# Optimization experiments

Measured on AMD Instinct MI355X. Metric: run time of the kernel, lower is better.

The kernel has to match this reference:

```python
import jax, jax.numpy as jnp
import numpy as np

B, N, C, H = 2, 2048, 1024, 16
D = C // H  # head_dim = 64


def _rope_freqs(n, d_half, theta=10000.0):
    inv = 1.0 / (theta ** (np.arange(0, d_half, dtype=np.float32) / d_half))
    ang = np.arange(n, dtype=np.float32)[:, None] * inv[None, :]
    return jnp.asarray(np.cos(ang)), jnp.asarray(np.sin(ang))


def setup_inputs() -> dict:
    key = jax.random.key(0)
    ks = jax.random.split(key, 5)
    cos, sin = _rope_freqs(N, D // 2)
    s = 0.02
    return {
        "x": jax.random.normal(ks[0], (B, N, C), jnp.float32),
        "w_qkv": jax.random.normal(ks[1], (3 * C, C), jnp.float32) * s,
        "b_qkv": jnp.zeros((3 * C,), jnp.float32),
        "w_proj": jax.random.normal(ks[2], (C, C), jnp.float32) * s,
        "b_proj": jnp.zeros((C,), jnp.float32),
        "freqs_cos": cos,
        "freqs_sin": sin,
    }


def _apply_rope(t, cos, sin):
    # t: (B, H, N, D); consecutive pairs (even, odd) form complex numbers,
    # matching torch.view_as_complex on reshape(..., D//2, 2).
    te = t[..., 0::2]
    to = t[..., 1::2]
    cos = cos[None, None, :, :]  # (1,1,N,D//2)
    sin = sin[None, None, :, :]
    oe = te * cos - to * sin
    oo = te * sin + to * cos
    return jnp.stack([oe, oo], axis=-1).reshape(t.shape)


def reference(x, w_qkv, b_qkv, w_proj, b_proj, freqs_cos, freqs_sin):
    b, n, c = x.shape
    qkv = x @ w_qkv.T + b_qkv                      # (B,N,3C)
    qkv = qkv.reshape(b, n, 3, H, D).transpose(2, 0, 3, 1, 4)  # (3,B,H,N,D)
    q, k, v = qkv[0], qkv[1], qkv[2]
    q = _apply_rope(q, freqs_cos, freqs_sin)
    k = _apply_rope(k, freqs_cos, freqs_sin)
    scale = 1.0 / jnp.sqrt(jnp.asarray(D, x.dtype))
    scores = jnp.einsum("bhqd,bhkd->bhqk", q, k) * scale
    attn = jax.nn.softmax(scores, axis=-1)
    out = jnp.einsum("bhqk,bhkd->bhqd", attn, v)   # (B,H,N,D)
    out = out.transpose(0, 2, 1, 3).reshape(b, n, c)
    return out @ w_proj.T + b_proj
```

## Files before the change

kernel.cpp:

```cpp
#include <hip/hip_runtime.h>
#include <hip/hip_bf16.h>
#include <stdint.h>

#define BB 2
#define NN 2048
#define CC 1024
#define HH 16
#define DD 64
#define C3 3072

typedef __attribute__((ext_vector_type(8))) short bf16x8;
typedef __attribute__((ext_vector_type(4))) short bf16x4;
typedef __attribute__((ext_vector_type(4))) float f32x4;
typedef __attribute__((ext_vector_type(16))) float f32x16;
typedef __attribute__((ext_vector_type(4))) unsigned short ushort4_t;

__device__ __forceinline__ unsigned short f2bf(float f) {
  union { float f; unsigned u; } v; v.f = f;
  unsigned r = v.u + 0x7FFFu + ((v.u >> 16) & 1u);
  return (unsigned short)(r >> 16);
}

#if __has_builtin(__builtin_amdgcn_exp2f)
#define EXP2(x) __builtin_amdgcn_exp2f(x)
#else
#define EXP2(x) exp2f(x)
#endif

__device__ __forceinline__ unsigned pack_bf2(float a, float b) {
  union { float f; unsigned u; } ua, ub; ua.f = a; ub.f = b;
#if __has_builtin(__builtin_amdgcn_perm)
  return __builtin_amdgcn_perm(ub.u, ua.u, 0x07060302u);
#else
  return (ua.u >> 16) | (ub.u & 0xFFFF0000u);
#endif
}

#define QSCALE 0.18033688f

#define GLDS(g, l) __builtin_amdgcn_global_load_lds( \
    (const __attribute__((address_space(1))) void*)(g), \
    (__attribute__((address_space(3))) void*)(l), 16, 0, 0)

__global__ __launch_bounds__(256) void k_cvt(
    const float* __restrict__ x, const float* __restrict__ wq,
    const float* __restrict__ wp,
    unsigned short* __restrict__ xb, unsigned short* __restrict__ wqb,
    unsigned short* __restrict__ wpb)
{
  int blk = blockIdx.x;
  const float* s; unsigned short* d; int i;
  if (blk < 4096)      { s = x;  d = xb;  i = blk * 256 + threadIdx.x; }
  else if (blk < 7168) { s = wq; d = wqb; i = (blk - 4096) * 256 + threadIdx.x; }
  else                 { s = wp; d = wpb; i = (blk - 7168) * 256 + threadIdx.x; }
  float4 v = ((const float4*)s)[i];
  ushort4_t o;
  o.x = f2bf(v.x); o.y = f2bf(v.y); o.z = f2bf(v.z); o.w = f2bf(v.w);
  ((ushort4_t*)d)[i] = o;
}

__global__ __launch_bounds__(256) void k_gemm_qkv(
    const unsigned short* __restrict__ A, const unsigned short* __restrict__ Bt,
    const float* __restrict__ bias,
    const float* __restrict__ cosb, const float* __restrict__ sinb,
    unsigned short* __restrict__ Qg, unsigned short* __restrict__ Kg,
    unsigned short* __restrict__ Vt)
{
  __shared__ __align__(16) unsigned short Sh[16384];
  const int tid  = threadIdx.x;
  const int lane = tid & 63;
  const int wave = tid >> 6;
  const int bm = blockIdx.y * 128;
  const int bn = blockIdx.x * 128;
  const int wm = (wave >> 1) * 64;
  const int wn = (wave & 1) * 64;
  const int frow = lane & 15;
  const int fk   = (lane >> 4) * 8;
  const int K = 1024;
  const int NIT = K / 32;

  f32x4 acc[4][4] = {};

  const int row0 = tid >> 2, cc0 = tid & 3;
  const int row1 = row0 + 64;
  const unsigned short* Arow0 = A  + (size_t)(bm + row0) * K + cc0 * 8;
  const unsigned short* Arow1 = A  + (size_t)(bm + row1) * K + cc0 * 8;
  const unsigned short* Brow0 = Bt + (size_t)(bn + row0) * K + cc0 * 8;
  const unsigned short* Brow1 = Bt + (size_t)(bn + row1) * K + cc0 * 8;

  GLDS(Arow0, Sh + (size_t)tid * 8);
  GLDS(Brow0, Sh + 4096 + (size_t)tid * 8);
  GLDS(Arow1, Sh + (size_t)(tid + 256) * 8);
  GLDS(Brow1, Sh + 4096 + (size_t)(tid + 256) * 8);

  for (int it = 0; it < NIT; ++it) {
    const int p = it & 1;
    const unsigned short* As = Sh + p * 8192;
    const unsigned short* Bs = As + 4096;
    __syncthreads();

    if (it + 1 < NIT) {
      const int k1 = (it + 1) * 32;
      unsigned short* An = Sh + (1 - p) * 8192;
      GLDS(Arow0 + k1, An + (size_t)tid * 8);
      GLDS(Brow0 + k1, An + 4096 + (size_t)tid * 8);
      GLDS(Arow1 + k1, An + (size_t)(tid + 256) * 8);
      GLDS(Brow1 + k1, An + 4096 + (size_t)(tid + 256) * 8);
    }

    bf16x8 af[4], bfr[4];
#pragma unroll
    for (int t = 0; t < 4; ++t) {
      af[t]  = *(const bf16x8*)(As + (wm + t * 16 + frow) * 32 + fk);
      bfr[t] = *(const bf16x8*)(Bs + (wn + t * 16 + frow) * 32 + fk);
    }
#pragma unroll
    for (int mt = 0; mt < 4; ++mt)
#pragma unroll
      for (int nt = 0; nt < 4; ++nt)
        acc[mt][nt] = __builtin_amdgcn_mfma_f32_16x16x32_bf16(af[mt], bfr[nt], acc[mt][nt], 0, 0, 0);
  }
  __syncthreads();

  const int er0  = (lane >> 4) * 4;
  const int ecol = lane & 15;
  const int region = bn >> 10;
  const int gcol0 = bn + wn;
  const int h  = (gcol0 >> 6) & 15;
  const int rowg0 = bm + wm;
  const int b  = rowg0 >> 11;
  const int n0 = rowg0 & (NN - 1);
  unsigned short* wt = Sh + wave * 4096;

#pragma unroll
  for (int nt = 0; nt < 4; ++nt) {
    const int c64 = nt * 16 + ecol;
    const float bv = bias[gcol0 + c64];
    const int ii  = c64 >> 1;
#pragma unroll
    for (int mt = 0; mt < 4; ++mt)
#pragma unroll
      for (int r = 0; r < 4; ++r) {
        const int ml = mt * 16 + er0 + r;
        const int n  = n0 + ml;
        float v = acc[mt][nt][r] + bv;
        float vp = __shfl_xor(v, 1, 64);
        if (region == 2) {
          wt[c64 * 64 + ((((ml >> 3) ^ (c64 & 7)) << 3) | (ml & 7))] = f2bf(v);
        } else {
          float cth = cosb[n * 32 + ii], sth = sinb[n * 32 + ii];
          float ov = (c64 & 1) ? (vp * sth + v * cth)
                               : (v * cth - vp * sth);
          if (region == 0) ov *= QSCALE;
          wt[ml * 64 + ((((c64 >> 3) ^ (ml & 7)) << 3) | (c64 & 7))] = f2bf(ov);
        }
      }
  }

  const int rr = lane >> 3, cc = lane & 7;
  if (region == 2) {
    unsigned short* dst = Vt + (size_t)(b * HH + h) * DD * NN + n0;
    const int q8a = (cc >> 1) * 2;
    const int q8b = q8a + 1;
    const int half = (cc & 1) * 4;
#pragma unroll
    for (int it = 0; it < 8; ++it) {
      int dl = it * 8 + rr;
      union { bf16x4 h[2]; bf16x8 w; } vv;
      vv.h[0] = *(const bf16x4*)(wt + dl * 64 + ((q8a ^ (dl & 7)) << 3) + half);
      vv.h[1] = *(const bf16x4*)(wt + dl * 64 + ((q8b ^ (dl & 7)) << 3) + half);
      *(bf16x8*)(dst + (size_t)dl * NN + cc * 8) = vv.w;
    }
  } else {
    unsigned short* dqk = ((region == 0) ? Qg : Kg) +
                          ((size_t)(b * HH + h) * NN + n0) * DD;
#pragma unroll
    for (int it = 0; it < 8; ++it) {
      int ml = it * 8 + rr;
      bf16x8 vv = *(const bf16x8*)(wt + ml * 64 + ((cc ^ (ml & 7)) << 3));
      *(bf16x8*)(dqk + (size_t)ml * DD + cc * 8) = vv;
    }
  }
}

__global__ __launch_bounds__(256) void k_attn(
    const unsigned short* __restrict__ Qg, const unsigned short* __restrict__ Kg,
    const unsigned short* __restrict__ Vtg, unsigned short* __restrict__ Og)
{
  __shared__ __align__(16) unsigned short Ks[2][64 * 64];
  __shared__ __align__(16) unsigned short Vs[2][64 * 64];

  const int tid  = threadIdx.x;
  const int lane = tid & 63;
  const int wave = tid >> 6;
  const int bh = blockIdx.x >> 4;
  const int qt = blockIdx.x & 15;
  const int q0 = qt * 128 + wave * 32;
  const int l31 = lane & 31;
  const int hi  = lane >> 5;
  const int s7  = l31 & 7;

  const unsigned short* Qb = Qg  + (size_t)bh * NN * DD;
  const unsigned short* Kb = Kg  + (size_t)bh * NN * DD;
  const unsigned short* Vb = Vtg + (size_t)bh * DD * NN;

  int soffB[4];
#pragma unroll
  for (int i = 0; i < 4; ++i)
    soffB[i] = (l31 * 64 + (((2 * i + hi) ^ s7) << 3)) * 2;
  const char* KsB = (const char*)Ks;
  const char* VsB = (const char*)Vs;

  bf16x8 qf[4];
#pragma unroll
  for (int dc = 0; dc < 4; ++dc)
    qf[dc] = *(const bf16x8*)(Qb + (size_t)(q0 + l31) * DD + dc * 16 + hi * 8);

  bf16x8 ones;
#pragma unroll
  for (int i = 0; i < 8; ++i) ones[i] = (short)0x3F80;

  f32x16 oacc[2] = {};
  f32x16 lacc = {};

  const int row0 = tid >> 3, cc0 = tid & 7;
  const int sw0 = (cc0 ^ (row0 & 7)) * 8;

  GLDS(Kb + (size_t)row0 * DD + sw0,        Ks[0] + (size_t)tid * 8);
  GLDS(Vb + (size_t)row0 * NN + sw0,        Vs[0] + (size_t)tid * 8);
  GLDS(Kb + (size_t)(row0 + 32) * DD + sw0, Ks[0] + (size_t)(tid + 256) * 8);
  GLDS(Vb + (size_t)(row0 + 32) * NN + sw0, Vs[0] + (size_t)(tid + 256) * 8);

#pragma unroll 2
  for (int t = 0; t < NN / 64; ++t) {
    const int p = t & 1;
    __syncthreads();

    if (t + 1 < NN / 64) {
      const int j = (t + 1) * 64;
      GLDS(Kb + (size_t)(j + row0) * DD + sw0,      Ks[1 - p] + (size_t)tid * 8);
      GLDS(Vb + (size_t)row0 * NN + j + sw0,        Vs[1 - p] + (size_t)tid * 8);
      GLDS(Kb + (size_t)(j + row0 + 32) * DD + sw0, Ks[1 - p] + (size_t)(tid + 256) * 8);
      GLDS(Vb + (size_t)(row0 + 32) * NN + j + sw0, Vs[1 - p] + (size_t)(tid + 256) * 8);
    }

    f32x16 sacc[2] = {};
    __builtin_amdgcn_s_setprio(1);
#pragma unroll
    for (int T = 0; T < 2; ++T)
#pragma unroll
      for (int dc = 0; dc < 4; ++dc) {
        bf16x8 kf = *(const bf16x8*)(KsB + p * 8192 + T * 4096 + soffB[dc]);
        sacc[T] = __builtin_amdgcn_mfma_f32_32x32x16_bf16(kf, qf[dc], sacc[T], 0, 0, 0);
      }
    __builtin_amdgcn_s_setprio(0);

#pragma unroll
    for (int T = 0; T < 2; ++T) {
      unsigned pk[8];
#pragma unroll
      for (int jj = 0; jj < 8; ++jj) {
        float e0 = EXP2(sacc[T][2 * jj]);
        float e1 = EXP2(sacc[T][2 * jj + 1]);
        pk[jj] = pack_bf2(e0, e1);
      }
      union { unsigned u[4]; bf16x8 v; } fa, fb;
      fa.u[0] = pk[0]; fa.u[1] = pk[1]; fa.u[2] = pk[2]; fa.u[3] = pk[3];
      fb.u[0] = pk[4]; fb.u[1] = pk[5]; fb.u[2] = pk[6]; fb.u[3] = pk[7];
      __builtin_amdgcn_s_setprio(1);
#pragma unroll
      for (int dt = 0; dt < 2; ++dt) {
        bf16x8 v0 = *(const bf16x8*)(VsB + p * 8192 + dt * 4096 + soffB[2 * T + 0]);
        bf16x8 v1 = *(const bf16x8*)(VsB + p * 8192 + dt * 4096 + soffB[2 * T + 1]);
        oacc[dt] = __builtin_amdgcn_mfma_f32_32x32x16_bf16(fa.v, v0, oacc[dt], 0, 0, 0);
        oacc[dt] = __builtin_amdgcn_mfma_f32_32x32x16_bf16(fb.v, v1, oacc[dt], 0, 0, 0);
      }
      lacc = __builtin_amdgcn_mfma_f32_32x32x16_bf16(fa.v, ones, lacc, 0, 0, 0);
      lacc = __builtin_amdgcn_mfma_f32_32x32x16_bf16(fb.v, ones, lacc, 0, 0, 0);
      __builtin_amdgcn_s_setprio(0);
    }
  }

  const int b = bh >> 4;
  const int h = bh & 15;
#pragma unroll
  for (int r = 0; r < 16; ++r) {
    const int qr = (r & 3) + 8 * (r >> 2) + 4 * hi;
    const float linv = 1.0f / lacc[r];
    unsigned short* orow = Og + (size_t)(b * NN + q0 + qr) * CC + h * DD + l31;
    orow[0]  = f2bf(oacc[0][r] * linv);
    orow[32] = f2bf(oacc[1][r] * linv);
  }
}

__global__ __launch_bounds__(256) void k_gemm_proj(
    const unsigned short* __restrict__ A, const unsigned short* __restrict__ Bt,
    const float* __restrict__ bias, float* __restrict__ Co)
{
  __shared__ __align__(16) unsigned short As[2][64 * 32];
  __shared__ __align__(16) unsigned short Bs[2][128 * 32];
  const int tid  = threadIdx.x;
  const int lane = tid & 63;
  const int wave = tid >> 6;
  const int bm = blockIdx.y * 64;
  const int bn = blockIdx.x * 128;
  const int wm = (wave >> 1) * 32;
  const int wn = (wave & 1) * 64;
  const int frow = lane & 15;
  const int fk   = (lane >> 4) * 8;
  const int K = 1024;
  const int NIT = K / 32;

  f32x4 acc[2][4] = {};

  const int row0 = tid >> 2, cc0 = tid & 3;
  const unsigned short* Arow  = A  + (size_t)(bm + row0) * K + cc0 * 8;
  const unsigned short* Brow0 = Bt + (size_t)(bn + row0) * K + cc0 * 8;
  const unsigned short* Brow1 = Bt + (size_t)(bn + row0 + 64) * K + cc0 * 8;

  GLDS(Arow,  As[0] + (size_t)tid * 8);
  GLDS(Brow0, Bs[0] + (size_t)tid * 8);
  GLDS(Brow1, Bs[0] + (size_t)(tid + 256) * 8);

  for (int it = 0; it < NIT; ++it) {
    const int p = it & 1;
    __syncthreads();

    if (it + 1 < NIT) {
      const int k1 = (it + 1) * 32;
      GLDS(Arow  + k1, As[1 - p] + (size_t)tid * 8);
      GLDS(Brow0 + k1, Bs[1 - p] + (size_t)tid * 8);
      GLDS(Brow1 + k1, Bs[1 - p] + (size_t)(tid + 256) * 8);
    }

    bf16x8 af[2], bfr[4];
#pragma unroll
    for (int t = 0; t < 2; ++t)
      af[t] = *(const bf16x8*)(As[p] + (wm + t * 16 + frow) * 32 + fk);
#pragma unroll
    for (int t = 0; t < 4; ++t)
      bfr[t] = *(const bf16x8*)(Bs[p] + (wn + t * 16 + frow) * 32 + fk);
#pragma unroll
    for (int mt = 0; mt < 2; ++mt)
#pragma unroll
      for (int nt = 0; nt < 4; ++nt)
        acc[mt][nt] = __builtin_amdgcn_mfma_f32_16x16x32_bf16(af[mt], bfr[nt], acc[mt][nt], 0, 0, 0);
  }

  const int er0  = (lane >> 4) * 4;
  const int ecol = lane & 15;
#pragma unroll
  for (int nt = 0; nt < 4; ++nt) {
    int col = bn + wn + nt * 16 + ecol;
    float bv = bias[col];
#pragma unroll
    for (int mt = 0; mt < 2; ++mt)
#pragma unroll
      for (int r = 0; r < 4; ++r) {
        int rowg = bm + wm + mt * 16 + er0 + r;
        Co[(size_t)rowg * CC + col] = acc[mt][nt][r] + bv;
      }
  }
}

extern "C" void kernel_launch(void* const* d_in, const int* in_sizes, int n_in,
                              void* d_out, int out_size, void* d_ws, size_t ws_size,
                              hipStream_t stream)
{
  const float* x      = (const float*)d_in[0];
  const float* w_qkv  = (const float*)d_in[1];
  const float* b_qkv  = (const float*)d_in[2];
  const float* w_proj = (const float*)d_in[3];
  const float* b_proj = (const float*)d_in[4];
  const float* fcos   = (const float*)d_in[5];
  const float* fsin   = (const float*)d_in[6];
  float* out = (float*)d_out;

  char* ws = (char*)d_ws;
  unsigned short* xb     = (unsigned short*)(ws);
  unsigned short* wqkvb  = (unsigned short*)(ws + 8388608);
  unsigned short* wprojb = (unsigned short*)(ws + 14680064);
  unsigned short* Qb     = (unsigned short*)(ws + 16777216);
  unsigned short* Kb     = (unsigned short*)(ws + 25165824);
  unsigned short* Vtb    = (unsigned short*)(ws + 33554432);
  unsigned short* aob    = (unsigned short*)(ws + 41943040);

  k_cvt<<<8192, 256, 0, stream>>>(x, w_qkv, w_proj, xb, wqkvb, wprojb);

  k_gemm_qkv<<<dim3(24, 32), 256, 0, stream>>>(xb, wqkvb, b_qkv, fcos, fsin,
                                               Qb, Kb, Vtb);

  k_attn<<<512, 256, 0, stream>>>(Qb, Kb, Vtb, aob);

  k_gemm_proj<<<dim3(8, 64), 256, 0, stream>>>(aob, wprojb, b_proj, out);
}
```

Before: 200.8 us.

## Triple-buffer K/V tiles in attention with partial vmcnt waits

Switches the attention kernel's K/V staging from a double buffer to a three-deep ring, prefetching two tiles ahead. It waits on vmcnt(4) instead of draining all outstanding loads before each barrier, so the next tile's loads can stay in flight during compute. This is meant to hide global-to-LDS latency better. In exchange it uses 48KB of LDS per block instead of 32KB, which may lower occupancy. Buffer indices are now runtime ring counters and the loop is no longer unrolled by two.

```diff
diff --git a/kernel.cpp b/kernel.cpp
--- a/kernel.cpp
+++ b/kernel.cpp
@@ -187,8 +187,8 @@
     const unsigned short* __restrict__ Qg, const unsigned short* __restrict__ Kg,
     const unsigned short* __restrict__ Vtg, unsigned short* __restrict__ Og)
 {
-  __shared__ __align__(16) unsigned short Ks[2][64 * 64];
-  __shared__ __align__(16) unsigned short Vs[2][64 * 64];
+  __shared__ __align__(16) unsigned short Ks[3][64 * 64];
+  __shared__ __align__(16) unsigned short Vs[3][64 * 64];
 
   const int tid  = threadIdx.x;
   const int lane = tid & 63;
@@ -208,8 +208,6 @@
 #pragma unroll
   for (int i = 0; i < 4; ++i)
     soffB[i] = (l31 * 64 + (((2 * i + hi) ^ s7) << 3)) * 2;
-  const char* KsB = (const char*)Ks;
-  const char* VsB = (const char*)Vs;
 
   bf16x8 qf[4];
 #pragma unroll
@@ -226,23 +224,30 @@
   const int row0 = tid >> 3, cc0 = tid & 7;
   const int sw0 = (cc0 ^ (row0 & 7)) * 8;
 
-  GLDS(Kb + (size_t)row0 * DD + sw0,        Ks[0] + (size_t)tid * 8);
-  GLDS(Vb + (size_t)row0 * NN + sw0,        Vs[0] + (size_t)tid * 8);
-  GLDS(Kb + (size_t)(row0 + 32) * DD + sw0, Ks[0] + (size_t)(tid + 256) * 8);
-  GLDS(Vb + (size_t)(row0 + 32) * NN + sw0, Vs[0] + (size_t)(tid + 256) * 8);
-
-#pragma unroll 2
-  for (int t = 0; t < NN / 64; ++t) {
-    const int p = t & 1;
-    __syncthreads();
-
-    if (t + 1 < NN / 64) {
-      const int j = (t + 1) * 64;
-      GLDS(Kb + (size_t)(j + row0) * DD + sw0,      Ks[1 - p] + (size_t)tid * 8);
-      GLDS(Vb + (size_t)row0 * NN + j + sw0,        Vs[1 - p] + (size_t)tid * 8);
-      GLDS(Kb + (size_t)(j + row0 + 32) * DD + sw0, Ks[1 - p] + (size_t)(tid + 256) * 8);
-      GLDS(Vb + (size_t)(row0 + 32) * NN + j + sw0, Vs[1 - p] + (size_t)(tid + 256) * 8);
-    }
+#define STAGE_KV(bf, j) do { \
+    GLDS(Kb + (size_t)((j) + row0) * DD + sw0,      Ks[bf] + (size_t)tid * 8); \
+    GLDS(Vb + (size_t)row0 * NN + (j) + sw0,        Vs[bf] + (size_t)tid * 8); \
+    GLDS(Kb + (size_t)((j) + row0 + 32) * DD + sw0, Ks[bf] + (size_t)(tid + 256) * 8); \
+    GLDS(Vb + (size_t)(row0 + 32) * NN + (j) + sw0, Vs[bf] + (size_t)(tid + 256) * 8); \
+  } while (0)
+
+  STAGE_KV(0, 0);
+  STAGE_KV(1, 64);
+
+  int bc = 0;
+  int bs = 2;
+  const int NT = NN / 64;
+
+  for (int t = 0; t < NT; ++t) {
+    if (t == NT - 1) asm volatile("s_waitcnt vmcnt(0)" ::: "memory");
+    else             asm volatile("s_waitcnt vmcnt(4)" ::: "memory");
+    __builtin_amdgcn_s_barrier();
+    __builtin_amdgcn_sched_barrier(0);
+
+    if (t + 2 < NT) STAGE_KV(bs, (t + 2) * 64);
+
+    const char* KsB = (const char*)Ks[bc];
+    const char* VsB = (const char*)Vs[bc];
 
     f32x16 sacc[2] = {};
     __builtin_amdgcn_s_setprio(1);
@@ -250,7 +255,7 @@
     for (int T = 0; T < 2; ++T)
 #pragma unroll
       for (int dc = 0; dc < 4; ++dc) {
-        bf16x8 kf = *(const bf16x8*)(KsB + p * 8192 + T * 4096 + soffB[dc]);
+        bf16x8 kf = *(const bf16x8*)(KsB + T * 4096 + soffB[dc]);
         sacc[T] = __builtin_amdgcn_mfma_f32_32x32x16_bf16(kf, qf[dc], sacc[T], 0, 0, 0);
       }
     __builtin_amdgcn_s_setprio(0);
@@ -270,8 +275,8 @@
       __builtin_amdgcn_s_setprio(1);
 #pragma unroll
       for (int dt = 0; dt < 2; ++dt) {
-        bf16x8 v0 = *(const bf16x8*)(VsB + p * 8192 + dt * 4096 + soffB[2 * T + 0]);
-        bf16x8 v1 = *(const bf16x8*)(VsB + p * 8192 + dt * 4096 + soffB[2 * T + 1]);
+        bf16x8 v0 = *(const bf16x8*)(VsB + dt * 4096 + soffB[2 * T + 0]);
+        bf16x8 v1 = *(const bf16x8*)(VsB + dt * 4096 + soffB[2 * T + 1]);
         oacc[dt] = __builtin_amdgcn_mfma_f32_32x32x16_bf16(fa.v, v0, oacc[dt], 0, 0, 0);
         oacc[dt] = __builtin_amdgcn_mfma_f32_32x32x16_bf16(fb.v, v1, oacc[dt], 0, 0, 0);
       }
@@ -279,7 +284,11 @@
       lacc = __builtin_amdgcn_mfma_f32_32x32x16_bf16(fb.v, ones, lacc, 0, 0, 0);
       __builtin_amdgcn_s_setprio(0);
     }
-  }
+
+    bc = (bc == 2) ? 0 : bc + 1;
+    bs = (bs == 2) ? 0 : bs + 1;
+  }
+#undef STAGE_KV
 
   const int b = bh >> 4;
   const int h = bh & 15;
```

Result: slower. 205.1 us (+2.1%).
